# Optimization experiments

Measured on AMD Instinct MI355X. Metric: run time of the kernel, lower is better.

## Reference

```python
import jax, jax.numpy as jnp
import numpy as np

HEAD_DIM = 128
SCALE = HEAD_DIM ** -0.5  # head_scaling == up_scaling == 1/sqrt(head_dim)


def setup_inputs() -> dict:
    key = jax.random.key(0)
    kq, kk, ku, kv = jax.random.split(key, 4)
    B, H, S, D = 2, 16, 2048, 128
    Hk, I = 4, 2048
    Q = jax.random.normal(kq, (B, H, S, D), dtype=jnp.float32)
    K = jax.random.normal(kk, (Hk, I, D), dtype=jnp.float32)
    U = jax.random.normal(ku, (Hk, I, D), dtype=jnp.float32)
    V = jax.random.normal(kv, (Hk, I, D), dtype=jnp.float32)
    return {"Q": Q, "K": K, "U": U, "V": V}


def reference(Q, K, U, V):
    # Q: (B, H, S, D); K/U/V: (Hk, I, D); GQA grouping G = H // Hk
    B, H, S, D = Q.shape
    Hk, I, _ = K.shape
    G = H // Hk
    Qr = Q.reshape(B, Hk, G, S, D)
    # gate scores and up projection, both scaled by 1/sqrt(D)
    M = jnp.einsum('bkgsd,kid->bkgsi', Qr, K) * SCALE
    N = jnp.einsum('bkgsd,kid->bkgsi', Qr, U) * SCALE
    A = jax.nn.silu(M) * N  # gated activation, (B, Hk, G, S, I)
    out = jnp.einsum('bkgsi,kid->bkgsd', A, V)
    return out.reshape(B, H, S, D)
```

## Files before the change

kernel.cpp:

```cpp
#include <hip/hip_runtime.h>

#define B_   2
#define H_   16
#define G_   4
#define S_   2048
#define D_   128
#define I_   2048

#define BM   256
#define BN   64
#define TPB  512
#define NIT  (I_ / BN)

#define KUSZ (BN * 128)
#define VSZ  (D_ * 64)

#define KIDX(r,c) ((r)*128 + ((c) ^ (((r)&7)<<3)))
#define VIDX(d,c) ((d)*64  + ((c) ^ (((d)&7)<<3)))

static constexpr float SCALE = 0.08838834764831845f;

typedef __fp16   p2v  __attribute__((ext_vector_type(2)));
typedef _Float16 h8v  __attribute__((ext_vector_type(8)));
typedef float    f4v  __attribute__((ext_vector_type(4)));
typedef float    f16v __attribute__((ext_vector_type(16)));
typedef int      i4v  __attribute__((ext_vector_type(4)));

__device__ __forceinline__ int pkf16(float a, float b) {
    p2v t = __builtin_amdgcn_cvt_pkrtz(a, b);
    int r; __builtin_memcpy(&r, &t, 4); return r;
}

__global__ __launch_bounds__(TPB, 2) void flashmlp_kernel(
    const float* __restrict__ Qg, const float* __restrict__ Kg,
    const float* __restrict__ Ug, const float* __restrict__ Vg,
    float* __restrict__ Og)
{
    __shared__ _Float16 Ks[2 * KUSZ];
    __shared__ _Float16 Us[2 * KUSZ];
    __shared__ _Float16 Vt[2 * VSZ];

    const int bid   = blockIdx.x;
    const int xcd   = bid & 7;
    const int kh    = xcd >> 1;
    const int j     = ((bid >> 3) << 1) | (xcd & 1);
    const int stile = j & 7;
    const int bg    = j >> 3;
    const int b     = bg >> 2;
    const int g     = bg & 3;
    const int h     = kh * G_ + g;

    const int tid  = threadIdx.x;
    const int wave = tid >> 6;
    const int lane = tid & 63;
    const int l31  = lane & 31;
    const int hl   = lane >> 5;

    const size_t qbase  = ((size_t)(b * H_ + h) * S_ + (size_t)stile * BM) * D_;
    const size_t kvbase = (size_t)kh * I_ * D_;

    h8v qf[8];
    {
        const float* qp = Qg + qbase + (size_t)(wave * 32 + l31) * D_;
#pragma unroll
        for (int ks = 0; ks < 8; ++ks) {
            const float4 a = *(const float4*)(qp + ks * 16 + hl * 8);
            const float4 c = *(const float4*)(qp + ks * 16 + hl * 8 + 4);
            h8v v;
            p2v* v2 = (p2v*)&v;
            v2[0] = __builtin_amdgcn_cvt_pkrtz(a.x * SCALE, a.y * SCALE);
            v2[1] = __builtin_amdgcn_cvt_pkrtz(a.z * SCALE, a.w * SCALE);
            v2[2] = __builtin_amdgcn_cvt_pkrtz(c.x * SCALE, c.y * SCALE);
            v2[3] = __builtin_amdgcn_cvt_pkrtz(c.z * SCALE, c.w * SCALE);
            qf[ks] = v;
        }
    }

    f16v acc_o[4];
#pragma unroll
    for (int dt = 0; dt < 4; ++dt)
#pragma unroll
        for (int e = 0; e < 16; ++e)
            acc_o[dt][e] = 0.f;

    const int sr  = tid >> 3;
    const int sc  = (tid & 7) * 16;
    const int d0  = tid & 127;
    const int io4 = (tid >> 7) * 16;
    const float* kbp = Kg + kvbase + (size_t)sr * D_ + sc;
    const float* ubp = Ug + kvbase + (size_t)sr * D_ + sc;

    float4 kpre[4], upre[4];
    float  vpre[16];

#pragma unroll
    for (int g4 = 0; g4 < 4; ++g4) {
        kpre[g4] = *(const float4*)(kbp + g4 * 4);
        upre[g4] = *(const float4*)(ubp + g4 * 4);
    }
#pragma unroll
    for (int jj = 0; jj < 16; ++jj)
        vpre[jj] = Vg[kvbase + (size_t)(io4 + jj) * D_ + d0];
    {
        h8v kb[2], ub[2], vb[2];
        p2v* kb2 = (p2v*)kb; p2v* ub2 = (p2v*)ub; p2v* vb2 = (p2v*)vb;
#pragma unroll
        for (int g4 = 0; g4 < 4; ++g4) {
            kb2[2 * g4 + 0] = __builtin_amdgcn_cvt_pkrtz(kpre[g4].x, kpre[g4].y);
            kb2[2 * g4 + 1] = __builtin_amdgcn_cvt_pkrtz(kpre[g4].z, kpre[g4].w);
            ub2[2 * g4 + 0] = __builtin_amdgcn_cvt_pkrtz(upre[g4].x, upre[g4].y);
            ub2[2 * g4 + 1] = __builtin_amdgcn_cvt_pkrtz(upre[g4].z, upre[g4].w);
        }
#pragma unroll
        for (int jj = 0; jj < 8; ++jj)
            vb2[jj] = __builtin_amdgcn_cvt_pkrtz(vpre[2 * jj], vpre[2 * jj + 1]);
        *(h8v*)(&Ks[KIDX(sr, sc + 0)]) = kb[0];
        *(h8v*)(&Ks[KIDX(sr, sc + 8)]) = kb[1];
        *(h8v*)(&Us[KIDX(sr, sc + 0)]) = ub[0];
        *(h8v*)(&Us[KIDX(sr, sc + 8)]) = ub[1];
        *(h8v*)(&Vt[VIDX(d0, io4 + 0)]) = vb[0];
        *(h8v*)(&Vt[VIDX(d0, io4 + 8)]) = vb[1];
    }
    __syncthreads();

    for (int it = 0; it < NIT; ++it) {
        const int cur = it & 1;
        const _Float16* ksb = Ks + cur * KUSZ;
        const _Float16* usb = Us + cur * KUSZ;
        const _Float16* vtb = Vt + cur * VSZ;

        const bool more = (it + 1 < NIT);
        if (more) {
            const float* kp = kbp + (size_t)(it + 1) * BN * D_;
            const float* up = ubp + (size_t)(it + 1) * BN * D_;
#pragma unroll
            for (int g4 = 0; g4 < 4; ++g4) {
                kpre[g4] = *(const float4*)(kp + g4 * 4);
                upre[g4] = *(const float4*)(up + g4 * 4);
            }
            const float* vp = Vg + kvbase + (size_t)((it + 1) * BN + io4) * D_ + d0;
#pragma unroll
            for (int jj = 0; jj < 16; ++jj)
                vpre[jj] = vp[(size_t)jj * D_];
        }

        h8v pb[4];
#pragma unroll
        for (int t2 = 0; t2 < 2; ++t2) {
            f16v am, an;
#pragma unroll
            for (int e = 0; e < 16; ++e) { am[e] = 0.f; an[e] = 0.f; }
            __builtin_amdgcn_s_setprio(1);
#pragma unroll
            for (int ks = 0; ks < 8; ++ks) {
                const h8v kf = *(const h8v*)(&ksb[KIDX(t2 * 32 + l31, ks * 16 + hl * 8)]);
                const h8v uf = *(const h8v*)(&usb[KIDX(t2 * 32 + l31, ks * 16 + hl * 8)]);
                am = __builtin_amdgcn_mfma_f32_32x32x16_f16(kf, qf[ks], am, 0, 0, 0);
                an = __builtin_amdgcn_mfma_f32_32x32x16_f16(uf, qf[ks], an, 0, 0, 0);
            }
            __builtin_amdgcn_s_setprio(0);

            int P[8];
#pragma unroll
            for (int p = 0; p < 8; ++p) {
                const float m0 = am[2 * p + 0], n0 = an[2 * p + 0];
                const float m1 = am[2 * p + 1], n1 = an[2 * p + 1];
                const float g0 = m0 * __builtin_amdgcn_rcpf(1.f + __expf(-m0)) * n0;
                const float g1 = m1 * __builtin_amdgcn_rcpf(1.f + __expf(-m1)) * n1;
                P[p] = pkf16(g0, g1);
            }
            auto sA = __builtin_amdgcn_permlane32_swap(P[0], P[2], false, false);
            auto sB = __builtin_amdgcn_permlane32_swap(P[1], P[3], false, false);
            auto sC = __builtin_amdgcn_permlane32_swap(P[4], P[6], false, false);
            auto sD = __builtin_amdgcn_permlane32_swap(P[5], P[7], false, false);
            i4v wlo = i4v{static_cast<int>(sA[0]), static_cast<int>(sB[0]),
                          static_cast<int>(sA[1]), static_cast<int>(sB[1])};
            i4v whi = i4v{static_cast<int>(sC[0]), static_cast<int>(sD[0]),
                          static_cast<int>(sC[1]), static_cast<int>(sD[1])};
            __builtin_memcpy(&pb[2 * t2 + 0], &wlo, 16);
            __builtin_memcpy(&pb[2 * t2 + 1], &whi, 16);
        }

        if (more) {
            _Float16* ksn = Ks + (cur ^ 1) * KUSZ;
            _Float16* usn = Us + (cur ^ 1) * KUSZ;
            _Float16* vtn = Vt + (cur ^ 1) * VSZ;
            h8v kb[2], ub[2], vb[2];
            p2v* kb2 = (p2v*)kb; p2v* ub2 = (p2v*)ub; p2v* vb2 = (p2v*)vb;
#pragma unroll
            for (int g4 = 0; g4 < 4; ++g4) {
                kb2[2 * g4 + 0] = __builtin_amdgcn_cvt_pkrtz(kpre[g4].x, kpre[g4].y);
                kb2[2 * g4 + 1] = __builtin_amdgcn_cvt_pkrtz(kpre[g4].z, kpre[g4].w);
                ub2[2 * g4 + 0] = __builtin_amdgcn_cvt_pkrtz(upre[g4].x, upre[g4].y);
                ub2[2 * g4 + 1] = __builtin_amdgcn_cvt_pkrtz(upre[g4].z, upre[g4].w);
            }
#pragma unroll
            for (int jj = 0; jj < 8; ++jj)
                vb2[jj] = __builtin_amdgcn_cvt_pkrtz(vpre[2 * jj], vpre[2 * jj + 1]);
            *(h8v*)(&ksn[KIDX(sr, sc + 0)]) = kb[0];
            *(h8v*)(&ksn[KIDX(sr, sc + 8)]) = kb[1];
            *(h8v*)(&usn[KIDX(sr, sc + 0)]) = ub[0];
            *(h8v*)(&usn[KIDX(sr, sc + 8)]) = ub[1];
            *(h8v*)(&vtn[VIDX(d0, io4 + 0)]) = vb[0];
            *(h8v*)(&vtn[VIDX(d0, io4 + 8)]) = vb[1];
        }

#pragma unroll
        for (int ks2 = 0; ks2 < 4; ++ks2) {
            h8v va[4];
#pragma unroll
            for (int dt = 0; dt < 4; ++dt)
                va[dt] = *(const h8v*)(&vtb[VIDX(dt * 32 + l31, ks2 * 16 + hl * 8)]);
            __builtin_amdgcn_s_setprio(1);
#pragma unroll
            for (int dt = 0; dt < 4; ++dt)
                acc_o[dt] = __builtin_amdgcn_mfma_f32_32x32x16_f16(va[dt], pb[ks2], acc_o[dt], 0, 0, 0);
            __builtin_amdgcn_s_setprio(0);
        }

        __syncthreads();
    }

    {
        const int qrow = stile * BM + wave * 32 + l31;
        float* op = Og + ((size_t)(b * H_ + h) * S_ + qrow) * D_;
#pragma unroll
        for (int dt = 0; dt < 4; ++dt)
#pragma unroll
            for (int g4 = 0; g4 < 4; ++g4) {
                f4v v = f4v{acc_o[dt][4 * g4 + 0], acc_o[dt][4 * g4 + 1],
                            acc_o[dt][4 * g4 + 2], acc_o[dt][4 * g4 + 3]};
                *(f4v*)(op + dt * 32 + g4 * 8 + hl * 4) = v;
            }
    }
}

extern "C" void kernel_launch(void* const* d_in, const int* in_sizes, int n_in,
                              void* d_out, int out_size, void* d_ws, size_t ws_size,
                              hipStream_t stream) {
    const float* Q = (const float*)d_in[0];
    const float* K = (const float*)d_in[1];
    const float* U = (const float*)d_in[2];
    const float* V = (const float*)d_in[3];
    float* out = (float*)d_out;

    const int grid = (S_ / BM) * B_ * H_;
    flashmlp_kernel<<<dim3(grid), dim3(TPB), 0, stream>>>(Q, K, U, V, out);
}
```

Before: 200.3 us.

## Pre-convert K/U/V to swizzled fp16 tiles and stream via direct global-to-LDS loads

Adds a pre-pass kernel that converts K, U and V to fp16 once, already swizzled and with V transposed into the per-tile shared-memory layout, and writes them to the workspace. The main kernel then fills shared memory with global_load_lds DMA copies instead of fp32 register loads, per-thread conversion and LDS stores, which halves global bytes and cuts register and VALU pressure. The V-projection MFMAs are also interleaved into the gate loop for each 32-row half. The cost is an extra launch and a workspace round trip; the conversion is redone on every call.

```diff
diff --git a/kernel.cpp b/kernel.cpp
--- a/kernel.cpp
+++ b/kernel.cpp
@@ -11,9 +11,7 @@
 #define BN   64
 #define TPB  512
 #define NIT  (I_ / BN)
-
-#define KUSZ (BN * 128)
-#define VSZ  (D_ * 64)
+#define TSZ  8192
 
 #define KIDX(r,c) ((r)*128 + ((c) ^ (((r)&7)<<3)))
 #define VIDX(d,c) ((d)*64  + ((c) ^ (((d)&7)<<3)))
@@ -31,14 +29,74 @@
     int r; __builtin_memcpy(&r, &t, 4); return r;
 }
 
+#define GL_LDS(gp, lp) __builtin_amdgcn_global_load_lds(                      \
+    (const __attribute__((address_space(1))) void*)(gp),                      \
+    (__attribute__((address_space(3))) void*)(lp), 16, 0, 0)
+
+__global__ __launch_bounds__(256) void convert_kernel(
+    const float* __restrict__ Kg, const float* __restrict__ Ug,
+    const float* __restrict__ Vg, _Float16* __restrict__ ws)
+{
+    const int bid = blockIdx.x;
+    const int tid = threadIdx.x;
+    __shared__ float vt[64 * 128];
+    if (bid < 256) {
+        const int kh = bid >> 6, m = (bid >> 5) & 1, it = bid & 31;
+        const float* src = (m ? Ug : Kg) + (size_t)kh * I_ * D_ + (size_t)it * BN * D_;
+        _Float16* dst = ws + (((size_t)kh * 3 + m) * 32 + it) * TSZ;
+        const int r   = tid >> 2;
+        const int cb  = (tid & 3) * 32;
+        const int swz = (r & 7) << 3;
+#pragma unroll
+        for (int g = 0; g < 4; ++g) {
+            const int cc0 = cb + g * 8;
+            const int d0  = cc0 ^ swz;
+            const float4 a = *(const float4*)(src + r * D_ + d0);
+            const float4 c = *(const float4*)(src + r * D_ + d0 + 4);
+            h8v v; p2v* v2 = (p2v*)&v;
+            v2[0] = __builtin_amdgcn_cvt_pkrtz(a.x, a.y);
+            v2[1] = __builtin_amdgcn_cvt_pkrtz(a.z, a.w);
+            v2[2] = __builtin_amdgcn_cvt_pkrtz(c.x, c.y);
+            v2[3] = __builtin_amdgcn_cvt_pkrtz(c.z, c.w);
+            *(h8v*)(dst + r * 128 + cc0) = v;
+        }
+    } else {
+        const int v  = bid - 256;
+        const int kh = v >> 5, it = v & 31;
+        const float* src = Vg + (size_t)kh * I_ * D_ + (size_t)it * BN * D_;
+#pragma unroll
+        for (int p = 0; p < 8; ++p) {
+            const int idx = p * 256 + tid;
+            const int i   = idx >> 5;
+            const int d4  = (idx & 31) * 4;
+            *(float4*)(&vt[i * 128 + d4]) = *(const float4*)(src + (size_t)i * D_ + d4);
+        }
+        __syncthreads();
+        _Float16* dst = ws + (((size_t)kh * 3 + 2) * 32 + it) * TSZ;
+        const int d   = tid >> 1;
+        const int cb  = (tid & 1) * 32;
+        const int swz = (d & 7) << 3;
+#pragma unroll
+        for (int g = 0; g < 4; ++g) {
+            const int cc0 = cb + g * 8;
+            const int ib  = cc0 ^ swz;
+            h8v w; p2v* w2 = (p2v*)&w;
+#pragma unroll
+            for (int pr = 0; pr < 4; ++pr)
+                w2[pr] = __builtin_amdgcn_cvt_pkrtz(vt[(ib + 2 * pr) * 128 + d],
+                                                    vt[(ib + 2 * pr + 1) * 128 + d]);
+            *(h8v*)(dst + d * 64 + cc0) = w;
+        }
+    }
+}
+
 __global__ __launch_bounds__(TPB, 2) void flashmlp_kernel(
-    const float* __restrict__ Qg, const float* __restrict__ Kg,
-    const float* __restrict__ Ug, const float* __restrict__ Vg,
+    const float* __restrict__ Qg, const _Float16* __restrict__ ws,
     float* __restrict__ Og)
 {
-    __shared__ _Float16 Ks[2 * KUSZ];
-    __shared__ _Float16 Us[2 * KUSZ];
-    __shared__ _Float16 Vt[2 * VSZ];
+    __shared__ _Float16 Ks[2 * TSZ];
+    __shared__ _Float16 Us[2 * TSZ];
+    __shared__ _Float16 Vt[2 * TSZ];
 
     const int bid   = blockIdx.x;
     const int xcd   = bid & 7;
@@ -56,8 +114,13 @@
     const int l31  = lane & 31;
     const int hl   = lane >> 5;
 
-    const size_t qbase  = ((size_t)(b * H_ + h) * S_ + (size_t)stile * BM) * D_;
-    const size_t kvbase = (size_t)kh * I_ * D_;
+    const size_t qbase = ((size_t)(b * H_ + h) * S_ + (size_t)stile * BM) * D_;
+    const _Float16* wsK = ws + (size_t)kh * 3 * 32 * TSZ;
+    const _Float16* wsU = wsK + (size_t)32 * TSZ;
+    const _Float16* wsV = wsK + (size_t)64 * TSZ;
+
+    const int so = wave * 1024 + lane * 8;
+    const int su = wave * 1024;
 
     h8v qf[8];
     {
@@ -66,8 +129,7 @@
         for (int ks = 0; ks < 8; ++ks) {
             const float4 a = *(const float4*)(qp + ks * 16 + hl * 8);
             const float4 c = *(const float4*)(qp + ks * 16 + hl * 8 + 4);
-            h8v v;
-            p2v* v2 = (p2v*)&v;
+            h8v v; p2v* v2 = (p2v*)&v;
             v2[0] = __builtin_amdgcn_cvt_pkrtz(a.x * SCALE, a.y * SCALE);
             v2[1] = __builtin_amdgcn_cvt_pkrtz(a.z * SCALE, a.w * SCALE);
             v2[2] = __builtin_amdgcn_cvt_pkrtz(c.x * SCALE, c.y * SCALE);
@@ -83,68 +145,38 @@
         for (int e = 0; e < 16; ++e)
             acc_o[dt][e] = 0.f;
 
-    const int sr  = tid >> 3;
-    const int sc  = (tid & 7) * 16;
-    const int d0  = tid & 127;
-    const int io4 = (tid >> 7) * 16;
-    const float* kbp = Kg + kvbase + (size_t)sr * D_ + sc;
-    const float* ubp = Ug + kvbase + (size_t)sr * D_ + sc;
-
-    float4 kpre[4], upre[4];
-    float  vpre[16];
-
-#pragma unroll
-    for (int g4 = 0; g4 < 4; ++g4) {
-        kpre[g4] = *(const float4*)(kbp + g4 * 4);
-        upre[g4] = *(const float4*)(ubp + g4 * 4);
-    }
-#pragma unroll
-    for (int jj = 0; jj < 16; ++jj)
-        vpre[jj] = Vg[kvbase + (size_t)(io4 + jj) * D_ + d0];
     {
-        h8v kb[2], ub[2], vb[2];
-        p2v* kb2 = (p2v*)kb; p2v* ub2 = (p2v*)ub; p2v* vb2 = (p2v*)vb;
-#pragma unroll
-        for (int g4 = 0; g4 < 4; ++g4) {
-            kb2[2 * g4 + 0] = __builtin_amdgcn_cvt_pkrtz(kpre[g4].x, kpre[g4].y);
-            kb2[2 * g4 + 1] = __builtin_amdgcn_cvt_pkrtz(kpre[g4].z, kpre[g4].w);
-            ub2[2 * g4 + 0] = __builtin_amdgcn_cvt_pkrtz(upre[g4].x, upre[g4].y);
-            ub2[2 * g4 + 1] = __builtin_amdgcn_cvt_pkrtz(upre[g4].z, upre[g4].w);
-        }
-#pragma unroll
-        for (int jj = 0; jj < 8; ++jj)
-            vb2[jj] = __builtin_amdgcn_cvt_pkrtz(vpre[2 * jj], vpre[2 * jj + 1]);
-        *(h8v*)(&Ks[KIDX(sr, sc + 0)]) = kb[0];
-        *(h8v*)(&Ks[KIDX(sr, sc + 8)]) = kb[1];
-        *(h8v*)(&Us[KIDX(sr, sc + 0)]) = ub[0];
-        *(h8v*)(&Us[KIDX(sr, sc + 8)]) = ub[1];
-        *(h8v*)(&Vt[VIDX(d0, io4 + 0)]) = vb[0];
-        *(h8v*)(&Vt[VIDX(d0, io4 + 8)]) = vb[1];
+        const _Float16* kt = wsK;
+        const _Float16* ut = wsU;
+        const _Float16* vt = wsV;
+        GL_LDS(kt + so,       Ks + su);
+        GL_LDS(kt + so + 512, Ks + su + 512);
+        GL_LDS(ut + so,       Us + su);
+        GL_LDS(ut + so + 512, Us + su + 512);
+        GL_LDS(vt + so,       Vt + su);
+        GL_LDS(vt + so + 512, Vt + su + 512);
     }
     __syncthreads();
 
     for (int it = 0; it < NIT; ++it) {
         const int cur = it & 1;
-        const _Float16* ksb = Ks + cur * KUSZ;
-        const _Float16* usb = Us + cur * KUSZ;
-        const _Float16* vtb = Vt + cur * VSZ;
-
-        const bool more = (it + 1 < NIT);
-        if (more) {
-            const float* kp = kbp + (size_t)(it + 1) * BN * D_;
-            const float* up = ubp + (size_t)(it + 1) * BN * D_;
-#pragma unroll
-            for (int g4 = 0; g4 < 4; ++g4) {
-                kpre[g4] = *(const float4*)(kp + g4 * 4);
-                upre[g4] = *(const float4*)(up + g4 * 4);
-            }
-            const float* vp = Vg + kvbase + (size_t)((it + 1) * BN + io4) * D_ + d0;
-#pragma unroll
-            for (int jj = 0; jj < 16; ++jj)
-                vpre[jj] = vp[(size_t)jj * D_];
-        }
-
-        h8v pb[4];
+        const _Float16* ksb = Ks + cur * TSZ;
+        const _Float16* usb = Us + cur * TSZ;
+        const _Float16* vtb = Vt + cur * TSZ;
+
+        if (it + 1 < NIT) {
+            const int nb = (cur ^ 1) * TSZ;
+            const _Float16* kt = wsK + (size_t)(it + 1) * TSZ;
+            const _Float16* ut = wsU + (size_t)(it + 1) * TSZ;
+            const _Float16* vt = wsV + (size_t)(it + 1) * TSZ;
+            GL_LDS(kt + so,       Ks + nb + su);
+            GL_LDS(kt + so + 512, Ks + nb + su + 512);
+            GL_LDS(ut + so,       Us + nb + su);
+            GL_LDS(ut + so + 512, Us + nb + su + 512);
+            GL_LDS(vt + so,       Vt + nb + su);
+            GL_LDS(vt + so + 512, Vt + nb + su + 512);
+        }
+
 #pragma unroll
         for (int t2 = 0; t2 < 2; ++t2) {
             f16v am, an;
@@ -173,49 +205,30 @@
             auto sB = __builtin_amdgcn_permlane32_swap(P[1], P[3], false, false);
             auto sC = __builtin_amdgcn_permlane32_swap(P[4], P[6], false, false);
             auto sD = __builtin_amdgcn_permlane32_swap(P[5], P[7], false, false);
-            i4v wlo = i4v{static_cast<int>(sA[0]), static_cast<int>(sB[0]),
-                          static_cast<int>(sA[1]), static_cast<int>(sB[1])};
-            i4v whi = i4v{static_cast<int>(sC[0]), static_cast<int>(sD[0]),
-                          static_cast<int>(sC[1]), static_cast<int>(sD[1])};
-            __builtin_memcpy(&pb[2 * t2 + 0], &wlo, 16);
-            __builtin_memcpy(&pb[2 * t2 + 1], &whi, 16);
-        }
-
-        if (more) {
-            _Float16* ksn = Ks + (cur ^ 1) * KUSZ;
-            _Float16* usn = Us + (cur ^ 1) * KUSZ;
-            _Float16* vtn = Vt + (cur ^ 1) * VSZ;
-            h8v kb[2], ub[2], vb[2];
-            p2v* kb2 = (p2v*)kb; p2v* ub2 = (p2v*)ub; p2v* vb2 = (p2v*)vb;
-#pragma unroll
-            for (int g4 = 0; g4 < 4; ++g4) {
-                kb2[2 * g4 + 0] = __builtin_amdgcn_cvt_pkrtz(kpre[g4].x, kpre[g4].y);
-                kb2[2 * g4 + 1] = __builtin_amdgcn_cvt_pkrtz(kpre[g4].z, kpre[g4].w);
-                ub2[2 * g4 + 0] = __builtin_amdgcn_cvt_pkrtz(upre[g4].x, upre[g4].y);
-                ub2[2 * g4 + 1] = __builtin_amdgcn_cvt_pkrtz(upre[g4].z, upre[g4].w);
-            }
-#pragma unroll
-            for (int jj = 0; jj < 8; ++jj)
-                vb2[jj] = __builtin_amdgcn_cvt_pkrtz(vpre[2 * jj], vpre[2 * jj + 1]);
-            *(h8v*)(&ksn[KIDX(sr, sc + 0)]) = kb[0];
-            *(h8v*)(&ksn[KIDX(sr, sc + 8)]) = kb[1];
-            *(h8v*)(&usn[KIDX(sr, sc + 0)]) = ub[0];
-            *(h8v*)(&usn[KIDX(sr, sc + 8)]) = ub[1];
-            *(h8v*)(&vtn[VIDX(d0, io4 + 0)]) = vb[0];
-            *(h8v*)(&vtn[VIDX(d0, io4 + 8)]) = vb[1];
-        }
-
-#pragma unroll
-        for (int ks2 = 0; ks2 < 4; ++ks2) {
-            h8v va[4];
-#pragma unroll
-            for (int dt = 0; dt < 4; ++dt)
-                va[dt] = *(const h8v*)(&vtb[VIDX(dt * 32 + l31, ks2 * 16 + hl * 8)]);
-            __builtin_amdgcn_s_setprio(1);
-#pragma unroll
-            for (int dt = 0; dt < 4; ++dt)
-                acc_o[dt] = __builtin_amdgcn_mfma_f32_32x32x16_f16(va[dt], pb[ks2], acc_o[dt], 0, 0, 0);
-            __builtin_amdgcn_s_setprio(0);
+            h8v pb0, pb1;
+            {
+                i4v wlo = i4v{static_cast<int>(sA[0]), static_cast<int>(sB[0]),
+                              static_cast<int>(sA[1]), static_cast<int>(sB[1])};
+                i4v whi = i4v{static_cast<int>(sC[0]), static_cast<int>(sD[0]),
+                              static_cast<int>(sC[1]), static_cast<int>(sD[1])};
+                __builtin_memcpy(&pb0, &wlo, 16);
+                __builtin_memcpy(&pb1, &whi, 16);
+            }
+
+#pragma unroll
+            for (int k2 = 0; k2 < 2; ++k2) {
+                const int ks2 = t2 * 2 + k2;
+                const h8v pb = k2 ? pb1 : pb0;
+                h8v va[4];
+#pragma unroll
+                for (int dt = 0; dt < 4; ++dt)
+                    va[dt] = *(const h8v*)(&vtb[VIDX(dt * 32 + l31, ks2 * 16 + hl * 8)]);
+                __builtin_amdgcn_s_setprio(1);
+#pragma unroll
+                for (int dt = 0; dt < 4; ++dt)
+                    acc_o[dt] = __builtin_amdgcn_mfma_f32_32x32x16_f16(va[dt], pb, acc_o[dt], 0, 0, 0);
+                __builtin_amdgcn_s_setprio(0);
+            }
         }
 
         __syncthreads();
@@ -243,7 +256,8 @@
     const float* U = (const float*)d_in[2];
     const float* V = (const float*)d_in[3];
     float* out = (float*)d_out;
-
-    const int grid = (S_ / BM) * B_ * H_;
-    flashmlp_kernel<<<dim3(grid), dim3(TPB), 0, stream>>>(Q, K, U, V, out);
-}
+    _Float16* ws = (_Float16*)d_ws;
+
+    convert_kernel<<<dim3(384), dim3(256), 0, stream>>>(K, U, V, ws);
+    flashmlp_kernel<<<dim3((S_ / BM) * B_ * H_), dim3(TPB), 0, stream>>>(Q, ws, out);
+}
```

New measurement: 195.6 us. 2.4% less time.
